# Optimization experiments

Measured on AMD Instinct MI355X. Metric: run time of the kernel, lower is better.

## Reference

```python
import jax, jax.numpy as jnp
import numpy as np

B, T, H, DK, DV, HID = 2, 2048, 6, 256, 256, 2048
EPS = 1e-5


def setup_inputs() -> dict:
    key = jax.random.key(0)
    ks = jax.random.split(key, 12)
    sd = 0.02
    hidden_ab = jax.random.normal(ks[0], (B, T, HID), jnp.float32)
    hidden_g = jax.random.normal(ks[1], (B, T, HID), jnp.float32)
    q = jax.random.normal(ks[2], (B, T, H, DK), jnp.float32)
    k = jax.random.normal(ks[3], (B, T, H, DK), jnp.float32)
    v = jax.random.normal(ks[4], (B, T, H, DV), jnp.float32)
    b_w = jax.random.normal(ks[5], (H, HID), jnp.float32) * sd
    a_w = jax.random.normal(ks[6], (H, HID), jnp.float32) * sd
    g_w = jax.random.normal(ks[7], (H, HID), jnp.float32) * sd
    A_log = jnp.log(jax.random.uniform(ks[8], (H,), jnp.float32, 1.0, 16.0))
    dt = jnp.exp(jax.random.uniform(ks[9], (H,), jnp.float32)
                 * (np.log(0.1) - np.log(0.001)) + np.log(0.001))
    dt = jnp.clip(dt, 1e-4)
    dt_bias = dt + jnp.log(-jnp.expm1(-dt))
    norm_w = jnp.ones((DV,), jnp.float32)
    o_w = jax.random.normal(ks[10], (H, DV, DK), jnp.float32) * sd
    return dict(hidden_ab=hidden_ab, hidden_g=hidden_g, q=q, k=k, v=v,
                b_w=b_w, a_w=a_w, A_log=A_log, dt_bias=dt_bias,
                g_w=g_w, norm_w=norm_w, o_w=o_w)


def _l2norm(x):
    return x * jax.lax.rsqrt(jnp.sum(x * x, axis=-1, keepdims=True) + 1e-6)


def _gated_delta_rule(q, k, v, g, beta):
    # q,k: [B,T,H,DK]; v: [B,T,H,DV]; g,beta: [B,T,H]
    q = _l2norm(q) * (DK ** -0.5)
    k = _l2norm(k)
    # time-major for scan
    qT = jnp.swapaxes(q, 0, 1)
    kT = jnp.swapaxes(k, 0, 1)
    vT = jnp.swapaxes(v, 0, 1)
    gT = jnp.swapaxes(g, 0, 1)
    bT = jnp.swapaxes(beta, 0, 1)

    def step(S, xs):
        qt, kt, vt, gt, bt = xs  # [B,H,*]
        S = S * jnp.exp(gt)[..., None, None]            # gated decay
        pred = jnp.einsum('bhk,bhkv->bhv', kt, S)        # current prediction
        delta = (vt - pred) * bt[..., None]              # beta-scaled error
        S = S + jnp.einsum('bhk,bhv->bhkv', kt, delta)   # delta-rule update
        ot = jnp.einsum('bhk,bhkv->bhv', qt, S)
        return S, ot

    S0 = jnp.zeros((B, H, DK, DV), q.dtype)
    _, oT = jax.lax.scan(step, S0, (qT, kT, vT, gT, bT))
    return jnp.swapaxes(oT, 0, 1)  # [B,T,H,DV]


def reference(hidden_ab, hidden_g, q, k, v, b_w, a_w, A_log, dt_bias, g_w, norm_w, o_w):
    beta = jax.nn.sigmoid(jnp.einsum('bth,nh->btn', hidden_ab, b_w))        # [B,T,H]
    g = -jnp.exp(A_log) * jax.nn.softplus(
        jnp.einsum('bth,nh->btn', hidden_ab, a_w) + dt_bias)                 # [B,T,H]
    o = _gated_delta_rule(q, k, v, g, beta)                                  # [B,T,H,DV]
    # FusedRMSNormSwishGate with per-head scalar gate
    gate = jnp.einsum('bth,nh->btn', hidden_g, g_w)                          # [B,T,H]
    o_n = o * jax.lax.rsqrt(jnp.mean(o * o, axis=-1, keepdims=True) + EPS) * norm_w
    o_n = o_n * (gate * jax.nn.sigmoid(gate))[..., None]
    # GroupLinear per head: head_v_dim -> head_dim
    out = jnp.einsum('bthv,hvd->bthd', o_n, o_w).reshape(B, T, H * DK)
    return out
```

## Files before the change

### kernel.cpp

```cpp
#include <hip/hip_runtime.h>
#include <hip/hip_bf16.h>
#include <math.h>

#define B_ 2
#define T_ 2048
#define H_ 6
#define DK_ 256
#define DV_ 256
#define HID_ 2048
#define C_ 64
#define NC_ 32

typedef __attribute__((ext_vector_type(8))) short short8;
typedef __attribute__((ext_vector_type(4))) float f32x4;

__device__ __forceinline__ unsigned rnebf(float f) {
  unsigned u = __float_as_uint(f);
  return (u + 0x7fffu + ((u >> 16) & 1u)) >> 16;
}
__device__ __forceinline__ unsigned pkbf(float lo, float hi) {
  return rnebf(lo) | (rnebf(hi) << 16);
}
__device__ __forceinline__ float bf2f(unsigned u16v) {
  return __uint_as_float((u16v & 0xffffu) << 16);
}
__device__ __forceinline__ short8 u4_to_s8(uint4 u) {
  union { uint4 u; short8 s; } c; c.u = u; return c.s;
}

__device__ __forceinline__ void gload_lds16(const void* g, void* l) {
  __builtin_amdgcn_global_load_lds(
      (const __attribute__((address_space(1))) unsigned int*)g,
      (__attribute__((address_space(3))) unsigned int*)l, 16, 0, 0);
}

__device__ __forceinline__ short8 buildB(uint2 Pe, uint2 Po, int lg, int c16) {
  const int src0 = ((2 * (lg & 1)) << 4) | c16;
  const int src1 = src0 + 16;
  int e0 = __shfl((int)Pe.x, src0), o0 = __shfl((int)Po.x, src0);
  int e1 = __shfl((int)Pe.y, src0), o1 = __shfl((int)Po.y, src0);
  int e2 = __shfl((int)Pe.x, src1), o2 = __shfl((int)Po.x, src1);
  int e3 = __shfl((int)Pe.y, src1), o3 = __shfl((int)Po.y, src1);
  const bool lo2 = (lg < 2);
  union { int i[4]; short8 s; } u;
  u.i[0] = lo2 ? e0 : o0;
  u.i[1] = lo2 ? e1 : o1;
  u.i[2] = lo2 ? e2 : o2;
  u.i[3] = lo2 ? e3 : o3;
  return u.s;
}

__global__ __launch_bounds__(256) void gdn_projnorm_kernel(
    const float* __restrict__ hab, const float* __restrict__ hg,
    const float* __restrict__ b_w, const float* __restrict__ a_w,
    const float* __restrict__ g_w, const float* __restrict__ A_log,
    const float* __restrict__ dt_bias,
    float* __restrict__ beta_o, float* __restrict__ g_o,
    float* __restrict__ sgate_o,
    const float* __restrict__ q, const float* __restrict__ k,
    float* __restrict__ sq, float* __restrict__ sk) {
  const int tid = threadIdx.x;
  const int lane = tid & 63;
  const int wid = tid >> 6;

  if (blockIdx.x >= B_ * T_) {
    const int gw = (blockIdx.x - B_ * T_) * 4 + wid;
    const float4 qv = *(const float4*)(q + (size_t)gw * DK_ + lane * 4);
    const float4 kv = *(const float4*)(k + (size_t)gw * DK_ + lane * 4);
    float sums_q = qv.x * qv.x + qv.y * qv.y + qv.z * qv.z + qv.w * qv.w;
    float sums_k = kv.x * kv.x + kv.y * kv.y + kv.z * kv.z + kv.w * kv.w;
#pragma unroll
    for (int m = 1; m < 64; m <<= 1) {
      sums_q += __shfl_xor(sums_q, m);
      sums_k += __shfl_xor(sums_k, m);
    }
    if (lane == 0) {
      sq[gw] = rsqrtf(sums_q + 1e-6f) * 0.0625f;
      sk[gw] = rsqrtf(sums_k + 1e-6f);
    }
    return;
  }

  const int bt = blockIdx.x;
  const float* h1 = hab + (size_t)bt * HID_ + tid * 8;
  const float* h2 = hg + (size_t)bt * HID_ + tid * 8;
  const float4 xa = *(const float4*)(h1);
  const float4 xb = *(const float4*)(h1 + 4);
  const float4 ya = *(const float4*)(h2);
  const float4 yb = *(const float4*)(h2 + 4);

  float part[18];
#pragma unroll
  for (int n = 0; n < 6; ++n) {
    const float* wp = b_w + n * HID_ + tid * 8;
    const float4 w0 = *(const float4*)(wp);
    const float4 w1 = *(const float4*)(wp + 4);
    part[n] = xa.x * w0.x + xa.y * w0.y + xa.z * w0.z + xa.w * w0.w +
              xb.x * w1.x + xb.y * w1.y + xb.z * w1.z + xb.w * w1.w;
  }
#pragma unroll
  for (int n = 0; n < 6; ++n) {
    const float* wp = a_w + n * HID_ + tid * 8;
    const float4 w0 = *(const float4*)(wp);
    const float4 w1 = *(const float4*)(wp + 4);
    part[6 + n] = xa.x * w0.x + xa.y * w0.y + xa.z * w0.z + xa.w * w0.w +
                  xb.x * w1.x + xb.y * w1.y + xb.z * w1.z + xb.w * w1.w;
  }
#pragma unroll
  for (int n = 0; n < 6; ++n) {
    const float* wp = g_w + n * HID_ + tid * 8;
    const float4 w0 = *(const float4*)(wp);
    const float4 w1 = *(const float4*)(wp + 4);
    part[12 + n] = ya.x * w0.x + ya.y * w0.y + ya.z * w0.z + ya.w * w0.w +
                   yb.x * w1.x + yb.y * w1.y + yb.z * w1.z + yb.w * w1.w;
  }

  __shared__ float red[18][4];
#pragma unroll
  for (int i = 0; i < 18; ++i) {
    float x = part[i];
    x += __shfl_xor(x, 1);
    x += __shfl_xor(x, 2);
    x += __shfl_xor(x, 4);
    x += __shfl_xor(x, 8);
    x += __shfl_xor(x, 16);
    x += __shfl_xor(x, 32);
    if (lane == 0) red[i][wid] = x;
  }
  __syncthreads();

  if (tid < 18) {
    const float s = red[tid][0] + red[tid][1] + red[tid][2] + red[tid][3];
    if (tid < 6) {
      beta_o[(size_t)bt * H_ + tid] = 1.f / (1.f + __expf(-s));
    } else if (tid < 12) {
      const int n = tid - 6;
      const float x = s + dt_bias[n];
      const float sp = (x > 20.f) ? x : log1pf(__expf(x));
      g_o[(size_t)bt * H_ + n] = -__expf(A_log[n]) * sp;
    } else {
      const int n = tid - 12;
      sgate_o[(size_t)bt * H_ + n] = s / (1.f + __expf(-s));
    }
  }
}

__global__ __launch_bounds__(256) void gdn_cum_kernel(
    const float* __restrict__ g, float* __restrict__ Gc,
    float* __restrict__ lam) {
  const int bh = blockIdx.x;
  const int b = bh / H_, h = bh - b * H_;
  const int w = threadIdx.x >> 6, l = threadIdx.x & 63;
  for (int it = 0; it < 8; ++it) {
    const int nc = it * 4 + w;
    const int tg = nc * C_ + l;
    const size_t srow = ((size_t)b * T_ + tg) * H_ + h;
    float val = g[srow];
#pragma unroll
    for (int ofs = 1; ofs < 64; ofs <<= 1) {
      const float o = __shfl_up(val, ofs);
      if (l >= ofs) val += o;
    }
    Gc[(bh * NC_ + nc) * C_ + l] = val;
    if (l == 63) lam[bh * NC_ + nc] = __expf(val);
  }
}

__device__ __forceinline__ int swz4(int row, int c4) {
  return row * 256 + (((c4) ^ ((row >> 2) & 7)) << 2);
}
__device__ __forceinline__ int swzi(int row, int c) {
  return row * 256 + ((((c) >> 2) ^ ((row >> 2) & 7)) << 2) + ((c) & 3);
}

__global__ __launch_bounds__(256) void gdn_prep_kernel(
    const float* __restrict__ q, const float* __restrict__ k,
    const float* __restrict__ v, const float* __restrict__ beta,
    const float* __restrict__ sq, const float* __restrict__ sk,
    const float* __restrict__ Gc, uint2* __restrict__ wUp,
    ushort* __restrict__ wWp, ushort* __restrict__ wMp,
    ushort* __restrict__ wQd, ushort* __restrict__ wkT,
    const float* __restrict__ o_w, ushort* __restrict__ owT) {
  __shared__ __attribute__((aligned(16))) char smem[158720];

  const int bid = blockIdx.x;
  const int tid = threadIdx.x;

  if (bid >= 512) {
    const int b2 = bid - 512;
    const int h2 = b2 >> 2;
    const int db = (b2 & 3) * 64;
    ushort* t = (ushort*)smem;
#pragma unroll
    for (int it = 0; it < 16; ++it) {
      const int v2 = it * 16 + (tid >> 4);
      const int dl = 4 * (tid & 15);
      const float4 x =
          *(const float4*)&o_w[((size_t)h2 * 256 + v2) * 256 + db + dl];
      t[(dl + 0) * 264 + v2] = (ushort)rnebf(x.x);
      t[(dl + 1) * 264 + v2] = (ushort)rnebf(x.y);
      t[(dl + 2) * 264 + v2] = (ushort)rnebf(x.z);
      t[(dl + 3) * 264 + v2] = (ushort)rnebf(x.w);
    }
    __syncthreads();
#pragma unroll
    for (int it = 0; it < 8; ++it) {
      const int idx = it * 256 + tid;
      const int d = idx >> 5;
      const int vv = (idx & 31) * 8;
      uint4 o;
      o.x = *(uint*)&t[d * 264 + vv + 0]; o.y = *(uint*)&t[d * 264 + vv + 2];
      o.z = *(uint*)&t[d * 264 + vv + 4]; o.w = *(uint*)&t[d * 264 + vv + 6];
      *(uint4*)&owT[((size_t)h2 * 256 + db + d) * 256 + vv] = o;
    }
    return;
  }

  const int bhx = bid & 15;
  if (bhx >= B_ * H_) return;
  const int nc = bid >> 4;
  const int bh = bhx;
  const int b = bh / H_, h = bh - b * H_;
  const int w = tid >> 6, l = tid & 63;
  const int lg = l >> 4, c16 = l & 15;
  const int cidx = bh * NC_ + nc;

  float* r1 = (float*)smem;
  ushort* knB = (ushort*)smem;
  ushort* qnB = (ushort*)(smem + 32768);
  float* r2 = (float*)(smem + 65536);
  float* AlT = (float*)(smem + 131072);
  ushort* Msc = (ushort*)(smem + 148480);
  float* bG = (float*)(smem + 157696);
  float* bB = bG + 64;
  float* bSc = bG + 128;
  float* bWl = bG + 192;

  const size_t srow0 = ((size_t)b * T_ + nc * C_) * H_ + h;
  if (tid < C_) {
    const float gv = Gc[cidx * C_ + tid];
    bG[tid] = gv;
    const float bb = beta[srow0 + (size_t)tid * H_];
    bB[tid] = bb;
    bSc[tid] = __expf(Gc[cidx * C_ + C_ - 1] - gv);
    bWl[tid] = bb * __expf(gv);
  }
  __syncthreads();

#pragma unroll
  for (int rr = 0; rr < 16; ++rr) {
    const int row = rr * 4 + w;
    const size_t g0 = (srow0 + (size_t)row * H_) * DK_;
    const float skr = sk[srow0 + (size_t)row * H_];
    const float sqr = sq[srow0 + (size_t)row * H_];
    float4 kv = *(const float4*)(k + g0 + 4 * l);
    float4 qv = *(const float4*)(q + g0 + 4 * l);
    kv.x *= skr; kv.y *= skr; kv.z *= skr; kv.w *= skr;
    qv.x *= sqr; qv.y *= sqr; qv.z *= sqr; qv.w *= sqr;
    const int boff = row * 512 + ((8 * l) ^ ((row & 7) << 4));
    uint2 pk_, pq_;
    pk_.x = pkbf(kv.x, kv.y); pk_.y = pkbf(kv.z, kv.w);
    pq_.x = pkbf(qv.x, qv.y); pq_.y = pkbf(qv.z, qv.w);
    *(uint2*)((char*)knB + boff) = pk_;
    *(uint2*)((char*)qnB + boff) = pq_;
    const float qe = __expf(bG[row]);
    uint2 oq;
    oq.x = pkbf(qv.x * qe, qv.y * qe);
    oq.y = pkbf(qv.z * qe, qv.w * qe);
    *(uint2*)&wQd[(srow0 + (size_t)row * H_) * DK_ + 4 * l] = oq;
  }
  __syncthreads();

  {
    const int xorv = (c16 & 7) << 4;
    const int rowA = 16 * w + c16;
    uint4 aq[8], ak[8];
#pragma unroll
    for (int kt = 0; kt < 8; ++kt) {
      const int coff = (64 * kt + 16 * lg) ^ xorv;
      aq[kt] = *(const uint4*)((char*)qnB + rowA * 512 + coff);
      ak[kt] = *(const uint4*)((char*)knB + rowA * 512 + coff);
    }
    f32x4 accm[4], acca[4];
#pragma unroll
    for (int nt = 0; nt < 4; ++nt) {
      accm[nt] = (f32x4){0.f, 0.f, 0.f, 0.f};
      acca[nt] = (f32x4){0.f, 0.f, 0.f, 0.f};
    }
#pragma unroll
    for (int nt = 0; nt < 4; ++nt) {
      const int rowB = 16 * nt + c16;
#pragma unroll
      for (int kt = 0; kt < 8; ++kt) {
        const uint4 bk =
            *(const uint4*)((char*)knB + rowB * 512 + ((64 * kt + 16 * lg) ^ xorv));
        const short8 bkf = u4_to_s8(bk);
        accm[nt] = __builtin_amdgcn_mfma_f32_16x16x32_bf16(u4_to_s8(aq[kt]),
                                                           bkf, accm[nt], 0, 0, 0);
        acca[nt] = __builtin_amdgcn_mfma_f32_16x16x32_bf16(u4_to_s8(ak[kt]),
                                                           bkf, acca[nt], 0, 0, 0);
      }
    }
#pragma unroll
    for (int nt = 0; nt < 4; ++nt) {
#pragma unroll
      for (int r = 0; r < 4; ++r) {
        const int t = 16 * w + 4 * lg + r;
        const int i = 16 * nt + c16;
        const float eg = __expf(bG[t] - bG[i]);
        Msc[t * 72 + i] = (ushort)((i <= t) ? rnebf(accm[nt][r] * eg) : 0u);
        AlT[i * 68 + t] = (i < t) ? bB[t] * eg * acca[nt][r] : 0.f;
      }
    }
  }
  {
    const int d = tid;
#pragma unroll
    for (int e = 0; e < 8; ++e) {
      float vj[8];
#pragma unroll
      for (int j = 0; j < 8; ++j) {
        const int t = 8 * e + j;
        const float kv = bf2f(*(const ushort*)((char*)knB + t * 512 +
                                               ((2 * d) ^ ((t & 7) << 4))));
        vj[j] = kv;
        r2[swzi(t, d)] = kv * bWl[t];
      }
      uint4 o;
      o.x = pkbf(vj[0] * bSc[8 * e + 0], vj[1] * bSc[8 * e + 1]);
      o.y = pkbf(vj[2] * bSc[8 * e + 2], vj[3] * bSc[8 * e + 3]);
      o.z = pkbf(vj[4] * bSc[8 * e + 4], vj[5] * bSc[8 * e + 5]);
      o.w = pkbf(vj[6] * bSc[8 * e + 6], vj[7] * bSc[8 * e + 7]);
      *(uint4*)&wkT[((size_t)cidx * 256 + d) * C_ + 8 * e] = o;
    }
  }
  __syncthreads();

  {
    const int row = tid >> 2;
#pragma unroll
    for (int e = 0; e < 2; ++e) {
      const int col = ((tid & 3) * 2 + e) * 8;
      *(uint4*)&wMp[(size_t)cidx * C_ * C_ + row * C_ + col] =
          *(const uint4*)&Msc[row * 72 + col];
    }
  }
#pragma unroll
  for (int rr = 0; rr < 16; ++rr) {
    const int row = rr * 4 + w;
    const float bbr = bB[row];
    const size_t g0 = (srow0 + (size_t)row * H_) * DV_;
    float4 vv = *(const float4*)(v + g0 + 4 * l);
    vv.x *= bbr; vv.y *= bbr; vv.z *= bbr; vv.w *= bbr;
    *(float4*)&r1[swz4(row, l)] = vv;
  }
  __syncthreads();

#pragma unroll
  for (int tb = 0; tb < 8; ++tb) {
    float xu[8], xw[8];
#pragma unroll
    for (int e = 0; e < 8; ++e) {
      xu[e] = r1[swzi(8 * tb + e, tid)];
      xw[e] = r2[swzi(8 * tb + e, tid)];
    }
    for (int i = 0; i < 8 * tb; ++i) {
      const float xui = r1[swzi(i, tid)];
      const float xwi = r2[swzi(i, tid)];
      float av[8];
      *(float4*)&av[0] = *(float4*)&AlT[i * 68 + 8 * tb];
      *(float4*)&av[4] = *(float4*)&AlT[i * 68 + 8 * tb + 4];
#pragma unroll
      for (int e = 0; e < 8; ++e) {
        xu[e] = fmaf(-av[e], xui, xu[e]);
        xw[e] = fmaf(-av[e], xwi, xw[e]);
      }
    }
#pragma unroll
    for (int e = 1; e < 8; ++e)
#pragma unroll
      for (int m = 0; m < 7; ++m)
        if (m < e) {
          const float am = AlT[(8 * tb + m) * 68 + 8 * tb + e];
          xu[e] = fmaf(-am, xu[m], xu[e]);
          xw[e] = fmaf(-am, xw[m], xw[e]);
        }
#pragma unroll
    for (int e = 0; e < 8; ++e) {
      r1[swzi(8 * tb + e, tid)] = xu[e];
      r2[swzi(8 * tb + e, tid)] = xw[e];
    }
  }
  {
    ushort* wb = wWp + (size_t)cidx * C_ * 256;
    for (int row = 0; row < C_; ++row)
      wb[row * 256 + tid] = (ushort)rnebf(r2[swzi(row, tid)]);
    const int cbw = tid >> 4, c16s = tid & 15;
#pragma unroll
    for (int mt = 0; mt < 4; ++mt) {
#pragma unroll
      for (int lgi = 0; lgi < 4; ++lgi) {
        const int r0 = 16 * mt + 4 * lgi;
        uint2 val;
        val.x = pkbf(r1[swzi(r0 + 0, tid)], r1[swzi(r0 + 1, tid)]);
        val.y = pkbf(r1[swzi(r0 + 2, tid)], r1[swzi(r0 + 3, tid)]);
        wUp[(((size_t)cidx * 16 + cbw) * 4 + mt) * 64 + (lgi << 4) + c16s] = val;
      }
    }
  }
}

__global__ __launch_bounds__(128, 1) void gdn_seq_kernel(
    const ushort* __restrict__ wkT, const ushort* __restrict__ wWp,
    const uint2* __restrict__ wUp, const float* __restrict__ lam,
    uint2* __restrict__ wDP, uint2* __restrict__ wSP) {
  const int bid = blockIdx.x;
  const int cb = bid >> 4, bhx = bid & 15;
  if (bhx >= B_ * H_) return;
  const int bh = bhx;
  const int tid = threadIdx.x;
  const int kh = tid >> 6, l = tid & 63;
  const int lg = l >> 4, c16 = l & 15;
  const int xorv = (c16 & 7) << 4;

  __shared__ ushort sW[2][16384];
  __shared__ ushort sK[2][16384];
  __shared__ uint2 sU[2][256];
  __shared__ f32x4 sX[2][4][64];
  __shared__ float sLam[NC_];

  auto stage = [&](int pp, int cidx2) {
    const char* gw_ = (const char*)(wWp + (size_t)cidx2 * 16384);
#pragma unroll
    for (int j = 0; j < 16; ++j) {
      const int i = kh * 16 + j;
      const int row = 2 * i + (l >> 5);
      const int colb = ((l & 31) * 16) ^ ((row & 7) << 4);
      gload_lds16(gw_ + row * 512 + colb, (char*)&sW[pp][0] + i * 1024);
    }
    const char* gk_ = (const char*)(wkT + (size_t)cidx2 * 16384);
#pragma unroll
    for (int j = 0; j < 16; ++j) {
      const int i = kh * 16 + j;
      const int row = 8 * i + (l >> 3);
      const int colb = ((l & 7) * 16) ^ ((row & 7) << 4);
      gload_lds16(gk_ + row * 128 + colb, (char*)&sK[pp][0] + i * 1024);
    }
    const char* gu_ = (const char*)wUp + ((size_t)cidx2 * 16 + cb) * 2048;
    gload_lds16(gu_ + kh * 1024 + l * 16, (char*)&sU[pp][0] + kh * 1024);
  };

  f32x4 S[8];
#pragma unroll
  for (int m2 = 0; m2 < 8; ++m2) S[m2] = (f32x4){0.f, 0.f, 0.f, 0.f};

  stage(0, bh * NC_ + 0);
  stage(1, bh * NC_ + 1);
  if (tid < NC_) sLam[tid] = lam[bh * NC_ + tid];
  asm volatile("s_waitcnt lgkmcnt(0)" ::: "memory");
  __builtin_amdgcn_sched_barrier(0);
  __builtin_amdgcn_s_barrier();
  __builtin_amdgcn_sched_barrier(0);

  for (int nc = 0; nc < NC_; ++nc) {
    const int pp = nc & 1;
    const int cidx = bh * NC_ + nc;
    if (nc == 0)
      asm volatile("s_waitcnt vmcnt(33)" ::: "memory");
    else if (nc == NC_ - 1)
      asm volatile("s_waitcnt vmcnt(5)" ::: "memory");
    else
      asm volatile("s_waitcnt vmcnt(38)" ::: "memory");
    __builtin_amdgcn_sched_barrier(0);
    __builtin_amdgcn_s_barrier();
    __builtin_amdgcn_sched_barrier(0);

    uint2 P[8];
#pragma unroll
    for (int m2 = 0; m2 < 8; ++m2) {
      P[m2].x = pkbf(S[m2][0], S[m2][1]);
      P[m2].y = pkbf(S[m2][2], S[m2][3]);
    }
    {
      uint4* sp4 = (uint4*)(wSP + (((size_t)cidx * 16 + cb) * 64 + l) * 16 +
                            kh * 8);
#pragma unroll
      for (int i = 0; i < 4; ++i) {
        uint4 o; o.x = P[2 * i].x; o.y = P[2 * i].y;
        o.z = P[2 * i + 1].x; o.w = P[2 * i + 1].y;
        sp4[i] = o;
      }
    }

    f32x4 pe[4], po[4];
#pragma unroll
    for (int mt = 0; mt < 4; ++mt) {
      pe[mt] = (f32x4){0.f, 0.f, 0.f, 0.f};
      po[mt] = (f32x4){0.f, 0.f, 0.f, 0.f};
    }
    const char* sWb = (const char*)&sW[pp][0];
#pragma unroll
    for (int ktl = 0; ktl < 4; ++ktl) {
      const int kt = kh * 4 + ktl;
      const short8 Bf = buildB(P[2 * ktl], P[2 * ktl + 1], lg, c16);
      const int colb = (64 * kt + 16 * lg) ^ xorv;
#pragma unroll
      for (int mt = 0; mt < 4; ++mt) {
        const uint4 aw = *(const uint4*)(sWb + (16 * mt + c16) * 512 + colb);
        if (ktl & 1)
          po[mt] = __builtin_amdgcn_mfma_f32_16x16x32_bf16(u4_to_s8(aw), Bf,
                                                           po[mt], 0, 0, 0);
        else
          pe[mt] = __builtin_amdgcn_mfma_f32_16x16x32_bf16(u4_to_s8(aw), Bf,
                                                           pe[mt], 0, 0, 0);
      }
    }
    f32x4 pl[4];
#pragma unroll
    for (int mt = 0; mt < 4; ++mt) {
      pl[mt] = pe[mt] + po[mt];
      sX[kh][mt][l] = pl[mt];
    }
    asm volatile("s_waitcnt lgkmcnt(0)" ::: "memory");
    __builtin_amdgcn_sched_barrier(0);
    __builtin_amdgcn_s_barrier();
    __builtin_amdgcn_sched_barrier(0);

    uint2 DP[4];
#pragma unroll
    for (int mt = 0; mt < 4; ++mt) {
      const f32x4 pr = sX[kh ^ 1][mt][l];
      const uint2 uu = sU[pp][mt * 64 + l];
      const float d0 = bf2f(uu.x) - (pl[mt][0] + pr[0]);
      const float d1 = bf2f(uu.x >> 16) - (pl[mt][1] + pr[1]);
      const float d2 = bf2f(uu.y) - (pl[mt][2] + pr[2]);
      const float d3 = bf2f(uu.y >> 16) - (pl[mt][3] + pr[3]);
      DP[mt].x = pkbf(d0, d1);
      DP[mt].y = pkbf(d2, d3);
    }
    {
      uint4* dp4 = (uint4*)(wDP + (((size_t)cidx * 16 + cb) * 64 + l) * 4);
      uint4 od;
      if (kh == 0) { od.x = DP[0].x; od.y = DP[0].y; od.z = DP[1].x; od.w = DP[1].y; }
      else         { od.x = DP[2].x; od.y = DP[2].y; od.z = DP[3].x; od.w = DP[3].y; }
      dp4[kh] = od;
    }
    const float lamC = sLam[nc];
#pragma unroll
    for (int m2 = 0; m2 < 8; ++m2) {
      S[m2][0] *= lamC; S[m2][1] *= lamC; S[m2][2] *= lamC; S[m2][3] *= lamC;
    }
    const char* sKb = (const char*)&sK[pp][0];
#pragma unroll
    for (int kt2 = 0; kt2 < 2; ++kt2) {
      const short8 Bd = buildB(DP[2 * kt2], DP[2 * kt2 + 1], lg, c16);
      const int colb = (64 * kt2 + 16 * lg) ^ xorv;
#pragma unroll
      for (int m2 = 0; m2 < 8; ++m2) {
        const int m2g = kh * 8 + m2;
        const uint4 ak = *(const uint4*)(sKb + (16 * m2g + c16) * 128 + colb);
        S[m2] = __builtin_amdgcn_mfma_f32_16x16x32_bf16(u4_to_s8(ak), Bd,
                                                        S[m2], 0, 0, 0);
      }
    }
    __builtin_amdgcn_sched_barrier(0);
    __builtin_amdgcn_s_barrier();
    __builtin_amdgcn_sched_barrier(0);
    if (nc + 2 < NC_) stage(pp, cidx + 2);
    __builtin_amdgcn_sched_barrier(0);
  }
}

__global__ __launch_bounds__(256) void gdn_ofin_kernel(
    const ushort* __restrict__ wQd, const ushort* __restrict__ wMp,
    const uint2* __restrict__ wDP, const uint2* __restrict__ wSP,
    const float* __restrict__ sgate, const float* __restrict__ norm_w,
    const ushort* __restrict__ owT, float* __restrict__ out) {
  const int slot = blockIdx.x;
  const int bhx = slot & 15;
  if (bhx >= B_ * H_) return;
  const int nc = slot >> 4;
  const int bh = bhx;
  const int cidx = bh * NC_ + nc;
  const int b = bh / H_, h = bh - b * H_;
  const int tid = threadIdx.x;
  const int w = tid >> 6, l = tid & 63;
  const int lg = l >> 4, c16 = l & 15;
  const size_t t0 = (size_t)b * T_ + nc * C_;

  __shared__ ushort onl[64 * 256];
  __shared__ float red[64][4];
  __shared__ float rowf[64];

  f32x4 acc[4][4];
#pragma unroll
  for (int mt = 0; mt < 4; ++mt)
#pragma unroll
    for (int nt = 0; nt < 4; ++nt) acc[mt][nt] = (f32x4){0.f, 0.f, 0.f, 0.f};

#pragma unroll
  for (int nt = 0; nt < 4; ++nt) {
    const int cbwq = 4 * w + nt;
    uint2 SPl[16];
    const uint4* sp4 =
        (const uint4*)(wSP + (((size_t)cidx * 16 + cbwq) * 64 + l) * 16);
#pragma unroll
    for (int i = 0; i < 8; ++i) {
      const uint4 t4 = sp4[i];
      SPl[2 * i].x = t4.x; SPl[2 * i].y = t4.y;
      SPl[2 * i + 1].x = t4.z; SPl[2 * i + 1].y = t4.w;
    }
#pragma unroll
    for (int kt = 0; kt < 8; ++kt) {
      const short8 Bf = buildB(SPl[2 * kt], SPl[2 * kt + 1], lg, c16);
#pragma unroll
      for (int mt = 0; mt < 4; ++mt) {
        const uint4 aq = *(const uint4*)&wQd[((t0 + 16 * mt + c16) * H_ + h) *
                                                 (size_t)DK_ +
                                             32 * kt + 8 * lg];
        acc[mt][nt] = __builtin_amdgcn_mfma_f32_16x16x32_bf16(
            u4_to_s8(aq), Bf, acc[mt][nt], 0, 0, 0);
      }
    }
  }
  const ushort* Mb = wMp + (size_t)cidx * C_ * C_;
#pragma unroll
  for (int nt = 0; nt < 4; ++nt) {
    const int cbwq = 4 * w + nt;
    uint2 DPl[4];
    {
      const uint4* dp4 =
          (const uint4*)(wDP + (((size_t)cidx * 16 + cbwq) * 64 + l) * 4);
      const uint4 a0 = dp4[0], a1 = dp4[1];
      DPl[0].x = a0.x; DPl[0].y = a0.y; DPl[1].x = a0.z; DPl[1].y = a0.w;
      DPl[2].x = a1.x; DPl[2].y = a1.y; DPl[3].x = a1.z; DPl[3].y = a1.w;
    }
#pragma unroll
    for (int kt2 = 0; kt2 < 2; ++kt2) {
      const short8 Bf = buildB(DPl[2 * kt2], DPl[2 * kt2 + 1], lg, c16);
#pragma unroll
      for (int mt = 0; mt < 4; ++mt) {
        const uint4 am =
            *(const uint4*)&Mb[(16 * mt + c16) * C_ + 32 * kt2 + 8 * lg];
        acc[mt][nt] = __builtin_amdgcn_mfma_f32_16x16x32_bf16(
            u4_to_s8(am), Bf, acc[mt][nt], 0, 0, 0);
      }
    }
  }

  float ss[4][4];
#pragma unroll
  for (int mt = 0; mt < 4; ++mt)
#pragma unroll
    for (int r = 0; r < 4; ++r) {
      float s = acc[mt][0][r] * acc[mt][0][r];
      s = fmaf(acc[mt][1][r], acc[mt][1][r], s);
      s = fmaf(acc[mt][2][r], acc[mt][2][r], s);
      s = fmaf(acc[mt][3][r], acc[mt][3][r], s);
      s += __shfl_xor(s, 1);
      s += __shfl_xor(s, 2);
      s += __shfl_xor(s, 4);
      s += __shfl_xor(s, 8);
      ss[mt][r] = s;
    }
  if (c16 == 0) {
#pragma unroll
    for (int mt = 0; mt < 4; ++mt)
#pragma unroll
      for (int r = 0; r < 4; ++r) red[16 * mt + 4 * lg + r][w] = ss[mt][r];
  }
  __syncthreads();
  if (tid < 64) {
    const float ms =
        (red[tid][0] + red[tid][1] + red[tid][2] + red[tid][3]) * (1.f / DV_);
    const float sg = sgate[(t0 + tid) * H_ + h];
    rowf[tid] = rsqrtf(ms + 1e-5f) * sg;
  }
  __syncthreads();

  {
    char* onb = (char*)onl;
#pragma unroll
    for (int mt = 0; mt < 4; ++mt) {
      float rf[4];
#pragma unroll
      for (int r = 0; r < 4; ++r) rf[r] = rowf[16 * mt + 4 * lg + r];
#pragma unroll
      for (int nt = 0; nt < 4; ++nt) {
        const int c = (4 * w + nt) * 16 + c16;
        const float nwv = norm_w[c];
#pragma unroll
        for (int r = 0; r < 4; ++r) {
          const int row = 16 * mt + 4 * lg + r;
          const float v = acc[mt][nt][r] * rf[r] * nwv;
          *(ushort*)(onb + row * 512 + ((2 * c) ^ ((row & 7) << 4))) =
              (ushort)rnebf(v);
        }
      }
    }
  }
  __syncthreads();

  f32x4 acc2[4][4];
#pragma unroll
  for (int mt = 0; mt < 4; ++mt)
#pragma unroll
    for (int nt2 = 0; nt2 < 4; ++nt2)
      acc2[mt][nt2] = (f32x4){0.f, 0.f, 0.f, 0.f};
  {
    const char* onb = (const char*)onl;
#pragma unroll
    for (int kt = 0; kt < 8; ++kt) {
      uint4 af[4];
#pragma unroll
      for (int mt = 0; mt < 4; ++mt)
        af[mt] = *(const uint4*)(onb + (16 * mt + c16) * 512 +
                                 ((64 * kt + 16 * lg) ^ ((c16 & 7) << 4)));
#pragma unroll
      for (int nt2 = 0; nt2 < 4; ++nt2) {
        const uint4 bf = *(const uint4*)&owT[((size_t)h * 256 +
                                              (4 * w + nt2) * 16 + c16) *
                                                 256 +
                                             32 * kt + 8 * lg];
#pragma unroll
        for (int mt = 0; mt < 4; ++mt)
          acc2[mt][nt2] = __builtin_amdgcn_mfma_f32_16x16x32_bf16(
              u4_to_s8(af[mt]), u4_to_s8(bf), acc2[mt][nt2], 0, 0, 0);
      }
    }
  }
#pragma unroll
  for (int mt = 0; mt < 4; ++mt)
#pragma unroll
    for (int nt2 = 0; nt2 < 4; ++nt2)
#pragma unroll
      for (int r = 0; r < 4; ++r)
        out[((t0 + 16 * mt + 4 * lg + r) * H_ + h) * (size_t)DK_ +
            (4 * w + nt2) * 16 + c16] = acc2[mt][nt2][r];
}

extern "C" void kernel_launch(void* const* d_in, const int* in_sizes, int n_in,
                              void* d_out, int out_size, void* d_ws,
                              size_t ws_size, hipStream_t stream) {
  const float* hab = (const float*)d_in[0];
  const float* hg = (const float*)d_in[1];
  const float* q = (const float*)d_in[2];
  const float* k = (const float*)d_in[3];
  const float* v = (const float*)d_in[4];
  const float* b_w = (const float*)d_in[5];
  const float* a_w = (const float*)d_in[6];
  const float* A_log = (const float*)d_in[7];
  const float* dt_bias = (const float*)d_in[8];
  const float* g_w = (const float*)d_in[9];
  const float* norm_w = (const float*)d_in[10];
  const float* o_w = (const float*)d_in[11];
  float* out = (float*)d_out;

  float* ws = (float*)d_ws;
  const size_t NBT = (size_t)B_ * T_ * H_;
  float* w_beta = ws;
  float* w_g = ws + NBT;
  float* w_sg = ws + 2 * NBT;
  float* w_sq = ws + 3 * NBT;
  float* w_sk = ws + 4 * NBT;
  float* w_G = ws + 5 * NBT;
  float* w_lam = ws + 7 * NBT;
  ushort* w_Qd = (ushort*)(ws + 7 * NBT + 1024);
  ushort* w_kT = w_Qd + (size_t)12582912;
  ushort* w_W = w_kT + (size_t)6291456;
  ushort* w_M = w_W + (size_t)6291456;
  uint2* w_U = (uint2*)(w_M + (size_t)1572864);
  uint2* w_DP = w_U + (size_t)1572864;
  uint2* w_SP = w_DP + (size_t)1572864;
  ushort* w_owT = (ushort*)(w_SP + (size_t)6291456);

  hipLaunchKernelGGL(gdn_projnorm_kernel,
                     dim3(B_ * T_ + B_ * T_ * H_ / 4), dim3(256), 0, stream,
                     hab, hg, b_w, a_w, g_w, A_log, dt_bias, w_beta, w_g,
                     w_sg, q, k, w_sq, w_sk);
  hipLaunchKernelGGL(gdn_cum_kernel, dim3(B_ * H_), dim3(256), 0, stream,
                     w_g, w_G, w_lam);
  hipLaunchKernelGGL(gdn_prep_kernel, dim3(512 + 24), dim3(256), 0, stream,
                     q, k, v, w_beta, w_sq, w_sk, w_G, w_U, w_W, w_M,
                     w_Qd, w_kT, o_w, w_owT);
  hipLaunchKernelGGL(gdn_seq_kernel, dim3(256), dim3(128), 0, stream,
                     w_kT, w_W, w_U, w_lam, w_DP, w_SP);
  hipLaunchKernelGGL(gdn_ofin_kernel, dim3(512), dim3(256), 0, stream,
                     w_Qd, w_M, w_DP, w_SP, w_sg, norm_w, w_owT, out);
}
```

Measured before the change: 266.1 us.

## Fold q/k L2-norm scaling into prep kernel using MFMA Gram diagonals

Drops the separate q/k norm blocks from the projection kernel, which re-read all of q and k from global memory. The prep kernel now loads raw q/k, stores them as bf16, and takes the squared norms from the diagonals of the existing k·k^T MFMA plus a new q·q^T MFMA. The scale factors are then applied to the M, A, W, kT and Qd outputs. This saves a full read of q and k and the sq/sk workspace round trip. In exchange it costs an extra sync, slightly more shared memory, and norms computed from bf16-rounded values, which may shift accuracy.

```diff
diff --git a/kernel.cpp b/kernel.cpp
--- a/kernel.cpp
+++ b/kernel.cpp
@@ -50,38 +50,18 @@
   return u.s;
 }
 
-__global__ __launch_bounds__(256) void gdn_projnorm_kernel(
+__global__ __launch_bounds__(256) void gdn_proj_kernel(
     const float* __restrict__ hab, const float* __restrict__ hg,
     const float* __restrict__ b_w, const float* __restrict__ a_w,
     const float* __restrict__ g_w, const float* __restrict__ A_log,
     const float* __restrict__ dt_bias,
     float* __restrict__ beta_o, float* __restrict__ g_o,
-    float* __restrict__ sgate_o,
-    const float* __restrict__ q, const float* __restrict__ k,
-    float* __restrict__ sq, float* __restrict__ sk) {
+    float* __restrict__ sgate_o) {
+  const int bt = blockIdx.x;
   const int tid = threadIdx.x;
   const int lane = tid & 63;
   const int wid = tid >> 6;
 
-  if (blockIdx.x >= B_ * T_) {
-    const int gw = (blockIdx.x - B_ * T_) * 4 + wid;
-    const float4 qv = *(const float4*)(q + (size_t)gw * DK_ + lane * 4);
-    const float4 kv = *(const float4*)(k + (size_t)gw * DK_ + lane * 4);
-    float sums_q = qv.x * qv.x + qv.y * qv.y + qv.z * qv.z + qv.w * qv.w;
-    float sums_k = kv.x * kv.x + kv.y * kv.y + kv.z * kv.z + kv.w * kv.w;
-#pragma unroll
-    for (int m = 1; m < 64; m <<= 1) {
-      sums_q += __shfl_xor(sums_q, m);
-      sums_k += __shfl_xor(sums_k, m);
-    }
-    if (lane == 0) {
-      sq[gw] = rsqrtf(sums_q + 1e-6f) * 0.0625f;
-      sk[gw] = rsqrtf(sums_k + 1e-6f);
-    }
-    return;
-  }
-
-  const int bt = blockIdx.x;
   const float* h1 = hab + (size_t)bt * HID_ + tid * 8;
   const float* h2 = hg + (size_t)bt * HID_ + tid * 8;
   const float4 xa = *(const float4*)(h1);
@@ -176,12 +156,11 @@
 __global__ __launch_bounds__(256) void gdn_prep_kernel(
     const float* __restrict__ q, const float* __restrict__ k,
     const float* __restrict__ v, const float* __restrict__ beta,
-    const float* __restrict__ sq, const float* __restrict__ sk,
     const float* __restrict__ Gc, uint2* __restrict__ wUp,
     ushort* __restrict__ wWp, ushort* __restrict__ wMp,
     ushort* __restrict__ wQd, ushort* __restrict__ wkT,
     const float* __restrict__ o_w, ushort* __restrict__ owT) {
-  __shared__ __attribute__((aligned(16))) char smem[158720];
+  __shared__ __attribute__((aligned(16))) char smem[160000];
 
   const int bid = blockIdx.x;
   const int tid = threadIdx.x;
@@ -235,15 +214,16 @@
   float* bB = bG + 64;
   float* bSc = bG + 128;
   float* bWl = bG + 192;
+  float* bKg = bG + 256;
+  float* bQg = bG + 320;
+  float* bSk = bG + 384;
+  float* bSq = bG + 448;
+  float* bQe = bG + 512;
 
   const size_t srow0 = ((size_t)b * T_ + nc * C_) * H_ + h;
   if (tid < C_) {
-    const float gv = Gc[cidx * C_ + tid];
-    bG[tid] = gv;
-    const float bb = beta[srow0 + (size_t)tid * H_];
-    bB[tid] = bb;
-    bSc[tid] = __expf(Gc[cidx * C_ + C_ - 1] - gv);
-    bWl[tid] = bb * __expf(gv);
+    bG[tid] = Gc[cidx * C_ + tid];
+    bB[tid] = beta[srow0 + (size_t)tid * H_];
   }
   __syncthreads();
 
@@ -251,26 +231,18 @@
   for (int rr = 0; rr < 16; ++rr) {
     const int row = rr * 4 + w;
     const size_t g0 = (srow0 + (size_t)row * H_) * DK_;
-    const float skr = sk[srow0 + (size_t)row * H_];
-    const float sqr = sq[srow0 + (size_t)row * H_];
-    float4 kv = *(const float4*)(k + g0 + 4 * l);
-    float4 qv = *(const float4*)(q + g0 + 4 * l);
-    kv.x *= skr; kv.y *= skr; kv.z *= skr; kv.w *= skr;
-    qv.x *= sqr; qv.y *= sqr; qv.z *= sqr; qv.w *= sqr;
+    const float4 kv = *(const float4*)(k + g0 + 4 * l);
+    const float4 qv = *(const float4*)(q + g0 + 4 * l);
     const int boff = row * 512 + ((8 * l) ^ ((row & 7) << 4));
     uint2 pk_, pq_;
     pk_.x = pkbf(kv.x, kv.y); pk_.y = pkbf(kv.z, kv.w);
     pq_.x = pkbf(qv.x, qv.y); pq_.y = pkbf(qv.z, qv.w);
     *(uint2*)((char*)knB + boff) = pk_;
     *(uint2*)((char*)qnB + boff) = pq_;
-    const float qe = __expf(bG[row]);
-    uint2 oq;
-    oq.x = pkbf(qv.x * qe, qv.y * qe);
-    oq.y = pkbf(qv.z * qe, qv.w * qe);
-    *(uint2*)&wQd[(srow0 + (size_t)row * H_) * DK_ + 4 * l] = oq;
-  }
-  __syncthreads();
-
+  }
+  __syncthreads();
+
+  f32x4 accm[4], acca[4];
   {
     const int xorv = (c16 & 7) << 4;
     const int rowA = 16 * w + c16;
@@ -281,12 +253,12 @@
       aq[kt] = *(const uint4*)((char*)qnB + rowA * 512 + coff);
       ak[kt] = *(const uint4*)((char*)knB + rowA * 512 + coff);
     }
-    f32x4 accm[4], acca[4];
 #pragma unroll
     for (int nt = 0; nt < 4; ++nt) {
       accm[nt] = (f32x4){0.f, 0.f, 0.f, 0.f};
       acca[nt] = (f32x4){0.f, 0.f, 0.f, 0.f};
     }
+    f32x4 accq = (f32x4){0.f, 0.f, 0.f, 0.f};
 #pragma unroll
     for (int nt = 0; nt < 4; ++nt) {
       const int rowB = 16 * nt + c16;
@@ -302,14 +274,46 @@
       }
     }
 #pragma unroll
+    for (int kt = 0; kt < 8; ++kt) {
+      const short8 bq = u4_to_s8(aq[kt]);
+      accq = __builtin_amdgcn_mfma_f32_16x16x32_bf16(bq, bq, accq, 0, 0, 0);
+    }
+#pragma unroll
+    for (int r = 0; r < 4; ++r) {
+      if ((c16 >> 2) == lg && (c16 & 3) == r) {
+        bKg[16 * w + c16] = acca[w][r];
+        bQg[16 * w + c16] = accq[r];
+      }
+    }
+  }
+  __syncthreads();
+
+  if (tid < C_) {
+    const float gv = bG[tid];
+    const float gend = bG[C_ - 1];
+    const float skv = rsqrtf(bKg[tid] + 1e-6f);
+    const float sqv = rsqrtf(bQg[tid] + 1e-6f) * 0.0625f;
+    bSk[tid] = skv;
+    bSq[tid] = sqv;
+    bSc[tid] = __expf(gend - gv) * skv;
+    bWl[tid] = bB[tid] * __expf(gv) * skv;
+    bQe[tid] = sqv * __expf(gv);
+  }
+  __syncthreads();
+
+  {
+#pragma unroll
     for (int nt = 0; nt < 4; ++nt) {
 #pragma unroll
       for (int r = 0; r < 4; ++r) {
         const int t = 16 * w + 4 * lg + r;
         const int i = 16 * nt + c16;
         const float eg = __expf(bG[t] - bG[i]);
-        Msc[t * 72 + i] = (ushort)((i <= t) ? rnebf(accm[nt][r] * eg) : 0u);
-        AlT[i * 68 + t] = (i < t) ? bB[t] * eg * acca[nt][r] : 0.f;
+        const float ski = bSk[i];
+        Msc[t * 72 + i] =
+            (ushort)((i <= t) ? rnebf(accm[nt][r] * bSq[t] * ski * eg) : 0u);
+        AlT[i * 68 + t] =
+            (i < t) ? bB[t] * bSk[t] * ski * eg * acca[nt][r] : 0.f;
       }
     }
   }
@@ -333,6 +337,19 @@
       o.w = pkbf(vj[6] * bSc[8 * e + 6], vj[7] * bSc[8 * e + 7]);
       *(uint4*)&wkT[((size_t)cidx * 256 + d) * C_ + 8 * e] = o;
     }
+  }
+#pragma unroll
+  for (int rr = 0; rr < 16; ++rr) {
+    const int row = rr * 4 + w;
+    const float qe = bQe[row];
+    const uint2 pq =
+        *(const uint2*)((char*)qnB + row * 512 + ((8 * l) ^ ((row & 7) << 4)));
+    const float q0 = bf2f(pq.x), q1 = bf2f(pq.x >> 16);
+    const float q2 = bf2f(pq.y), q3 = bf2f(pq.y >> 16);
+    uint2 oq;
+    oq.x = pkbf(q0 * qe, q1 * qe);
+    oq.y = pkbf(q2 * qe, q3 * qe);
+    *(uint2*)&wQd[(srow0 + (size_t)row * H_) * DK_ + 4 * l] = oq;
   }
   __syncthreads();
 
@@ -761,8 +778,6 @@
   float* w_beta = ws;
   float* w_g = ws + NBT;
   float* w_sg = ws + 2 * NBT;
-  float* w_sq = ws + 3 * NBT;
-  float* w_sk = ws + 4 * NBT;
   float* w_G = ws + 5 * NBT;
   float* w_lam = ws + 7 * NBT;
   ushort* w_Qd = (ushort*)(ws + 7 * NBT + 1024);
@@ -774,15 +789,14 @@
   uint2* w_SP = w_DP + (size_t)1572864;
   ushort* w_owT = (ushort*)(w_SP + (size_t)6291456);
 
-  hipLaunchKernelGGL(gdn_projnorm_kernel,
-                     dim3(B_ * T_ + B_ * T_ * H_ / 4), dim3(256), 0, stream,
+  hipLaunchKernelGGL(gdn_proj_kernel, dim3(B_ * T_), dim3(256), 0, stream,
                      hab, hg, b_w, a_w, g_w, A_log, dt_bias, w_beta, w_g,
-                     w_sg, q, k, w_sq, w_sk);
+                     w_sg);
   hipLaunchKernelGGL(gdn_cum_kernel, dim3(B_ * H_), dim3(256), 0, stream,
                      w_g, w_G, w_lam);
   hipLaunchKernelGGL(gdn_prep_kernel, dim3(512 + 24), dim3(256), 0, stream,
-                     q, k, v, w_beta, w_sq, w_sk, w_G, w_U, w_W, w_M,
-                     w_Qd, w_kT, o_w, w_owT);
+                     q, k, v, w_beta, w_G, w_U, w_W, w_M, w_Qd, w_kT, o_w,
+                     w_owT);
   hipLaunchKernelGGL(gdn_seq_kernel, dim3(256), dim3(128), 0, stream,
                      w_kT, w_W, w_U, w_lam, w_DP, w_SP);
   hipLaunchKernelGGL(gdn_ofin_kernel, dim3(512), dim3(256), 0, stream,
```

After: 256.3 us. -3.7%, faster.
